# Optimization experiments

Measured on AMD Instinct MI355X. Metric: run time of the kernel, lower is better.

The kernel has to match this reference:

```python
import jax, jax.numpy as jnp
import numpy as np

N, E, D, L, G = 50000, 1600000, 128, 3, 64


def setup_inputs() -> dict:
    key = jax.random.key(0)
    ks = jax.random.split(key, 10)
    s = 1.0 / np.sqrt(D).astype(np.float32)
    X = jax.random.normal(ks[0], (N, D), jnp.float32)
    edge_index = jax.random.randint(ks[1], (2, E), 0, N, dtype=jnp.int32)
    edge_types = jax.random.randint(ks[2], (E,), 0, 2, dtype=jnp.int32)
    batch_ids = jnp.sort(jax.random.randint(ks[3], (N,), 0, G, dtype=jnp.int32))
    Wd = jax.random.uniform(ks[4], (L, D, D), jnp.float32, -s, s)
    bd = jax.random.uniform(ks[5], (L, D), jnp.float32, -s, s)
    Wc = jax.random.uniform(ks[6], (L, D, D), jnp.float32, -s, s)
    bc = jax.random.uniform(ks[7], (L, D), jnp.float32, -s, s)
    Ws = jax.random.uniform(ks[8], (L, D, D), jnp.float32, -s, s)
    bs = jax.random.uniform(ks[9], (L, D), jnp.float32, -s, s)
    return dict(X=X, Wd=Wd, bd=bd, Wc=Wc, bc=bc, Ws=Ws, bs=bs,
                edge_index=edge_index, edge_types=edge_types, batch_ids=batch_ids)


def reference(X, Wd, bd, Wc, bc, Ws, bs, edge_index, edge_types, batch_ids):
    src, dst = edge_index[0], edge_index[1]
    is_data = (edge_types == 0)[:, None]  # [E,1] edge-type selector
    for l in range(L):
        # Linear commutes with gather: compute node-level GEMMs once,
        # then per-edge gather + type select (same math as per-edge Linear).
        Xd = X @ Wd[l] + bd[l]            # [N,D] data-edge messages
        Xc = X @ Wc[l] + bc[l]            # [N,D] control-edge messages
        msg = jnp.where(is_data, Xd[src], Xc[src])      # [E,D]
        agg = jax.ops.segment_sum(msg, dst, num_segments=N)  # scatter-add
        X = jax.nn.relu(agg + X @ Ws[l] + bs[l])
    # global mean pool per graph
    sums = jax.ops.segment_sum(X, batch_ids, num_segments=G)
    cnts = jax.ops.segment_sum(jnp.ones((N,), X.dtype), batch_ids, num_segments=G)
    return sums / jnp.maximum(cnts, 1.0)[:, None]
```

## Files before the change

### kernel.cpp

```cpp
#include <hip/hip_runtime.h>
#include <hip/hip_fp16.h>

#define N_NODES 50000
#define N_EDGES 1600000
#define DIM     128
#define NLAYERS 3
#define NGRAPHS 64

#define NBUCK   196
#define CSR_BLKS 256
#define EPB     (N_EDGES / CSR_BLKS)
#define EITER   ((EPB + 255) / 256)

typedef _Float16 half8 __attribute__((ext_vector_type(8)));
typedef float    f32x4 __attribute__((ext_vector_type(4)));
typedef float    f32x2 __attribute__((ext_vector_type(2)));

#define LDK 136

__device__ __forceinline__ unsigned char f32_to_fp8(float v) {
    int q = __builtin_amdgcn_cvt_pk_fp8_f32(v, v, 0, false);
    return (unsigned char)(q & 0xFF);
}

__global__ __launch_bounds__(256) void setup_kernel(
        const float* __restrict__ X, __half* __restrict__ Xh,
        const float* __restrict__ Wd, const float* __restrict__ Wc,
        const float* __restrict__ Ws, __half* __restrict__ WT,
        float* __restrict__ sums, int* __restrict__ gcnt) {
    int i = blockIdx.x * 256 + threadIdx.x;
    if (i < N_NODES * DIM / 4) {
        float4 v = *(const float4*)(X + (size_t)i * 4);
        union { __half2 h2[2]; uint2 u; } pk;
        pk.h2[0] = __floats2half2_rn(v.x, v.y);
        pk.h2[1] = __floats2half2_rn(v.z, v.w);
        *(uint2*)(Xh + (size_t)i * 4) = pk.u;
    }
    if (i < 9 * DIM * DIM) {
        int k  = i & 127;
        int n  = (i >> 7) & 127;
        int lw = i >> 14;
        int l  = lw / 3, w = lw - 3 * l;
        const float* W = ((w == 0) ? Wd : (w == 1) ? Wc : Ws)
                         + (size_t)l * DIM * DIM;
        WT[i] = __float2half(W[k * DIM + n]);
    }
    if (i < NGRAPHS * DIM) sums[i] = 0.f;
    if (i < NGRAPHS) gcnt[i] = 0;
}

__global__ __launch_bounds__(256) void csr1_kernel(const int* __restrict__ dst,
                                                   int* __restrict__ cntmat) {
    __shared__ int hc[NBUCK];
    int tid = threadIdx.x;
    for (int i = tid; i < NBUCK; i += 256) hc[i] = 0;
    __syncthreads();
    int base = blockIdx.x * EPB;
#pragma unroll
    for (int i = 0; i < EITER; ++i) {
        int idx = i * 256 + tid;
        if (idx < EPB) atomicAdd(&hc[dst[base + idx] >> 8], 1);
    }
    __syncthreads();
    for (int i = tid; i < NBUCK; i += 256)
        cntmat[i * CSR_BLKS + blockIdx.x] = hc[i];
}

__global__ __launch_bounds__(256) void scanA_kernel(const int* __restrict__ cntmat,
                                                    int* __restrict__ exc,
                                                    int* __restrict__ btot) {
    __shared__ int sh[256];
    int tid = threadIdx.x, b = blockIdx.x;
    int v = cntmat[b * CSR_BLKS + tid];
    sh[tid] = v;
    __syncthreads();
    for (int o = 1; o < 256; o <<= 1) {
        int t = (tid >= o) ? sh[tid - o] : 0;
        __syncthreads();
        sh[tid] += t;
        __syncthreads();
    }
    exc[b * CSR_BLKS + tid] = sh[tid] - v;
    if (tid == 255) btot[b] = sh[255];
}

__global__ __launch_bounds__(256) void csr2_kernel(const int* __restrict__ src,
                                                   const int* __restrict__ dst,
                                                   const int* __restrict__ et,
                                                   const int* __restrict__ exc,
                                                   const int* __restrict__ btot,
                                                   int* __restrict__ bstart,
                                                   int* __restrict__ esv) {
    __shared__ int sh[256];
    __shared__ int bst[NBUCK];
    __shared__ int cur[NBUCK];
    int tid = threadIdx.x;
    int v = (tid < NBUCK) ? btot[tid] : 0;
    sh[tid] = v;
    __syncthreads();
    for (int o = 1; o < 256; o <<= 1) {
        int t = (tid >= o) ? sh[tid - o] : 0;
        __syncthreads();
        sh[tid] += t;
        __syncthreads();
    }
    if (tid < NBUCK) bst[tid] = sh[tid] - v;
    if (blockIdx.x == 0) {
        if (tid < NBUCK) bstart[tid] = sh[tid] - v;
        if (tid == NBUCK - 1) bstart[NBUCK] = sh[tid];
    }
    __syncthreads();
    if (tid < NBUCK) cur[tid] = exc[tid * CSR_BLKS + blockIdx.x] + bst[tid];
    __syncthreads();
    int base = blockIdx.x * EPB;
#pragma unroll
    for (int i = 0; i < EITER; ++i) {
        int idx = i * 256 + tid;
        if (idx < EPB) {
            int e = base + idx;
            int d = dst[e];
            int pos = atomicAdd(&cur[d >> 8], 1);
            esv[pos] = (src[e] + et[e] * N_NODES) | ((d & 255) << 17);
        }
    }
}

__global__ __launch_bounds__(256) void csr3_kernel(const int* __restrict__ esv,
                                                   const int* __restrict__ bstart,
                                                   int* __restrict__ col,
                                                   int* __restrict__ row_start,
                                                   int* __restrict__ deg) {
    __shared__ int cnt[256];
    __shared__ int sh[256];
    __shared__ int cur[256];
    int tid = threadIdx.x, b = blockIdx.x;
    int bs = bstart[b], be = bstart[b + 1];
    cnt[tid] = 0;
    __syncthreads();
    for (int e = bs + tid; e < be; e += 256)
        atomicAdd(&cnt[(esv[e] >> 17) & 255], 1);
    __syncthreads();
    int v = cnt[tid];
    sh[tid] = v;
    __syncthreads();
    for (int o = 1; o < 256; o <<= 1) {
        int t = (tid >= o) ? sh[tid - o] : 0;
        __syncthreads();
        sh[tid] += t;
        __syncthreads();
    }
    int off  = sh[tid] - v;
    int node = (b << 8) + tid;
    if (node < N_NODES) {
        row_start[node] = bs + off;
        deg[node]       = v;
    }
    cur[tid] = bs + off;
    __syncthreads();
    for (int e = bs + tid; e < be; e += 256) {
        int pk  = esv[e];
        int nd  = (pk >> 17) & 255;
        int pos = atomicAdd(&cur[nd], 1);
        col[pos] = pk & 0x1FFFF;
    }
}

__global__ __launch_bounds__(256) void gemm3m_kernel(
        const __half* __restrict__ Xh,
        const __half* __restrict__ WTl,
        const float* __restrict__ bd, const float* __restrict__ bc,
        const float* __restrict__ bs,
        unsigned char* __restrict__ Od, unsigned char* __restrict__ Oc,
        __half* __restrict__ Sh) {
    __shared__ _Float16 As[64 * LDK];
    __shared__ _Float16 Bs[128 * LDK];

    const int tid = threadIdx.x;
    const int m0  = blockIdx.x * 64;
    const int w   = blockIdx.y;

#pragma unroll
    for (int i = 0; i < 4; ++i) {
        int c    = i * 256 + tid;
        int row  = c >> 4;
        int colh = (c & 15) * 8;
        uint4 v  = make_uint4(0u, 0u, 0u, 0u);
        int gr   = m0 + row;
        if (gr < N_NODES) v = *(const uint4*)(Xh + (size_t)gr * DIM + colh);
        *(uint4*)(As + row * LDK + colh) = v;
    }
    {
        const __half* Wt = WTl + (size_t)w * DIM * DIM;
#pragma unroll
        for (int i = 0; i < 8; ++i) {
            int c    = i * 256 + tid;
            int row  = c >> 4;
            int colh = (c & 15) * 8;
            uint4 v = *(const uint4*)(Wt + (size_t)row * DIM + colh);
            *(uint4*)(Bs + row * LDK + colh) = v;
        }
    }
    __syncthreads();

    const int wv = tid >> 6;
    const int l  = tid & 63;
    const int lm = l & 15;
    const int q  = l >> 4;

    const float* bias = (w == 0) ? bd : (w == 1) ? bc : bs;
    float b0v = bias[wv * 32 + lm];
    float b1v = bias[wv * 32 + 16 + lm];
    f32x4 acc[4][2];
#pragma unroll
    for (int mt = 0; mt < 4; ++mt) {
        acc[mt][0] = (f32x4){b0v, b0v, b0v, b0v};
        acc[mt][1] = (f32x4){b1v, b1v, b1v, b1v};
    }

#pragma unroll
    for (int ks = 0; ks < 4; ++ks) {
        int coff = ks * 32 + q * 8;
        half8 am[4];
#pragma unroll
        for (int mt = 0; mt < 4; ++mt)
            am[mt] = *(const half8*)(As + (mt * 16 + lm) * LDK + coff);
        half8 bb0 = *(const half8*)(Bs + (wv * 32 + lm) * LDK + coff);
        half8 bb1 = *(const half8*)(Bs + (wv * 32 + 16 + lm) * LDK + coff);
#pragma unroll
        for (int mt = 0; mt < 4; ++mt) {
            acc[mt][0] = __builtin_amdgcn_mfma_f32_16x16x32_f16(am[mt], bb0, acc[mt][0], 0, 0, 0);
            acc[mt][1] = __builtin_amdgcn_mfma_f32_16x16x32_f16(am[mt], bb1, acc[mt][1], 0, 0, 0);
        }
    }

    if (w < 2) {
        unsigned char* O = (w == 0) ? Od : Oc;
#pragma unroll
        for (int mt = 0; mt < 4; ++mt)
#pragma unroll
            for (int nt = 0; nt < 2; ++nt) {
                int colg = wv * 32 + nt * 16 + lm;
#pragma unroll
                for (int r = 0; r < 4; ++r) {
                    int row = m0 + mt * 16 + q * 4 + r;
                    if (row < N_NODES)
                        O[(size_t)row * DIM + colg] = f32_to_fp8(acc[mt][nt][r]);
                }
            }
    } else {
#pragma unroll
        for (int mt = 0; mt < 4; ++mt)
#pragma unroll
            for (int nt = 0; nt < 2; ++nt) {
                int colg = wv * 32 + nt * 16 + lm;
#pragma unroll
                for (int r = 0; r < 4; ++r) {
                    int row = m0 + mt * 16 + q * 4 + r;
                    if (row < N_NODES)
                        Sh[(size_t)row * DIM + colg] = __float2half(acc[mt][nt][r]);
                }
            }
    }
}

__global__ __launch_bounds__(256) void agg_kernel(
        const int* __restrict__ row_start, const int* __restrict__ deg_arr,
        const int* __restrict__ col,
        const unsigned char* __restrict__ Xdc,
        const __half* __restrict__ Sh, __half* __restrict__ Xout) {
    int wave = (blockIdx.x * 256 + threadIdx.x) >> 6;
    int lane = threadIdx.x & 63;
    int half = lane >> 5;
    int l32  = lane & 31;
    int node = wave * 2 + half;
    if (node >= N_NODES) return;

    int rs  = row_start[node];
    int deg = deg_arr[node];
    const size_t off = (size_t)l32 * 4;

    float4 a[8];
#pragma unroll
    for (int i = 0; i < 8; ++i) a[i] = make_float4(0.f, 0.f, 0.f, 0.f);

    if (deg > 0) {
        int dgm1 = deg - 1;
        int nb   = (deg + 7) >> 3;
        for (int b = 0; b < nb; ++b) {
            int e0 = b * 8;
            int p[8];
#pragma unroll
            for (int i = 0; i < 8; ++i) {
                int idx = e0 + i;
                p[i] = col[rs + (idx < deg ? idx : dgm1)];
            }
            unsigned int v[8];
#pragma unroll
            for (int i = 0; i < 8; ++i)
                v[i] = *(const unsigned int*)(Xdc + (size_t)p[i] * DIM + off);
#pragma unroll
            for (int i = 0; i < 8; ++i) {
                if (e0 + i >= deg) v[i] = 0u;
            }
#pragma unroll
            for (int i = 0; i < 8; ++i) {
                f32x2 f0 = __builtin_amdgcn_cvt_pk_f32_fp8(v[i], false);
                f32x2 f1 = __builtin_amdgcn_cvt_pk_f32_fp8(v[i], true);
                a[i].x += f0[0]; a[i].y += f0[1];
                a[i].z += f1[0]; a[i].w += f1[1];
            }
        }
    }

#pragma unroll
    for (int i = 1; i < 8; ++i) {
        a[0].x += a[i].x; a[0].y += a[i].y;
        a[0].z += a[i].z; a[0].w += a[i].w;
    }

    union { uint2 u; __half2 h2[2]; } sv;
    sv.u = *(const uint2*)(Sh + (size_t)node * DIM + off);
    float2 s0 = __half22float2(sv.h2[0]);
    float2 s1 = __half22float2(sv.h2[1]);

    float rx = fmaxf(a[0].x + s0.x, 0.f);
    float ry = fmaxf(a[0].y + s0.y, 0.f);
    float rz = fmaxf(a[0].z + s1.x, 0.f);
    float rw = fmaxf(a[0].w + s1.y, 0.f);

    union { __half2 h2[2]; uint2 u; } pk;
    pk.h2[0] = __floats2half2_rn(rx, ry);
    pk.h2[1] = __floats2half2_rn(rz, rw);
    *(uint2*)(Xout + (size_t)node * DIM + off) = pk.u;
}

__global__ __launch_bounds__(256) void pool_kernel(const __half* __restrict__ X,
                                                   const int* __restrict__ bid,
                                                   float* __restrict__ sums,
                                                   int* __restrict__ gcnt) {
    __shared__ float acc[8][DIM];
    __shared__ int scnt[8];
    __shared__ int sgmin;
    int tid = threadIdx.x;
    for (int i = tid; i < 8 * DIM; i += 256) ((float*)acc)[i] = 0.f;
    if (tid < 8) scnt[tid] = 0;
    int n0 = blockIdx.x * 64;
    if (tid == 0) sgmin = bid[n0];
    __syncthreads();
    int gmin = sgmin;

    int s    = tid >> 5;
    int lane = tid & 31;
    int r0   = n0 + s * 8;

    int g[8];
    union { uint2 u; __half2 h2[2]; } v[8];
#pragma unroll
    for (int i = 0; i < 8; ++i) {
        int r = r0 + i;
        g[i] = (r < N_NODES) ? bid[r] : -1;
    }
#pragma unroll
    for (int i = 0; i < 8; ++i) {
        int r = r0 + i;
        if (r < N_NODES)
            v[i].u = *(const uint2*)(X + (size_t)r * DIM + lane * 4);
        else { v[i].u.x = 0u; v[i].u.y = 0u; }
    }

    float4 a = make_float4(0.f, 0.f, 0.f, 0.f);
    int cur = -1, run = 0;
#pragma unroll
    for (int i = 0; i < 8; ++i) {
        if (g[i] != cur) {
            if (cur >= 0) {
                int slot = cur - gmin;
                if (slot < 8) {
                    atomicAdd(&acc[slot][lane * 4 + 0], a.x);
                    atomicAdd(&acc[slot][lane * 4 + 1], a.y);
                    atomicAdd(&acc[slot][lane * 4 + 2], a.z);
                    atomicAdd(&acc[slot][lane * 4 + 3], a.w);
                    if (lane == 0) atomicAdd(&scnt[slot], run);
                } else {
                    atomicAdd(&sums[cur * DIM + lane * 4 + 0], a.x);
                    atomicAdd(&sums[cur * DIM + lane * 4 + 1], a.y);
                    atomicAdd(&sums[cur * DIM + lane * 4 + 2], a.z);
                    atomicAdd(&sums[cur * DIM + lane * 4 + 3], a.w);
                    if (lane == 0) atomicAdd(&gcnt[cur], run);
                }
            }
            cur = g[i];
            a = make_float4(0.f, 0.f, 0.f, 0.f);
            run = 0;
        }
        if (g[i] >= 0) {
            float2 f0 = __half22float2(v[i].h2[0]);
            float2 f1 = __half22float2(v[i].h2[1]);
            a.x += f0.x; a.y += f0.y; a.z += f1.x; a.w += f1.y;
            run++;
        }
    }
    if (cur >= 0) {
        int slot = cur - gmin;
        if (slot < 8) {
            atomicAdd(&acc[slot][lane * 4 + 0], a.x);
            atomicAdd(&acc[slot][lane * 4 + 1], a.y);
            atomicAdd(&acc[slot][lane * 4 + 2], a.z);
            atomicAdd(&acc[slot][lane * 4 + 3], a.w);
            if (lane == 0) atomicAdd(&scnt[slot], run);
        } else {
            atomicAdd(&sums[cur * DIM + lane * 4 + 0], a.x);
            atomicAdd(&sums[cur * DIM + lane * 4 + 1], a.y);
            atomicAdd(&sums[cur * DIM + lane * 4 + 2], a.z);
            atomicAdd(&sums[cur * DIM + lane * 4 + 3], a.w);
            if (lane == 0) atomicAdd(&gcnt[cur], run);
        }
    }
    __syncthreads();

    for (int slot = 0; slot < 8; ++slot) {
        if (scnt[slot] > 0) {
            int gg = gmin + slot;
            for (int i = tid; i < DIM; i += 256)
                atomicAdd(&sums[gg * DIM + i], acc[slot][i]);
            if (tid == 0) atomicAdd(&gcnt[gg], scnt[slot]);
        }
    }
}

__global__ __launch_bounds__(256) void div_kernel(const float* __restrict__ sums,
                                                  const int* __restrict__ gcnt,
                                                  float* __restrict__ out) {
    int i = blockIdx.x * 256 + threadIdx.x;
    if (i < NGRAPHS * DIM) {
        int g = i >> 7;
        out[i] = sums[i] / fmaxf((float)gcnt[g], 1.f);
    }
}

extern "C" void kernel_launch(void* const* d_in, const int* in_sizes, int n_in,
                              void* d_out, int out_size, void* d_ws, size_t ws_size,
                              hipStream_t stream) {
    const float* Xin = (const float*)d_in[0];
    const float* Wd  = (const float*)d_in[1];
    const float* bd  = (const float*)d_in[2];
    const float* Wc  = (const float*)d_in[3];
    const float* bc  = (const float*)d_in[4];
    const float* Ws  = (const float*)d_in[5];
    const float* bs  = (const float*)d_in[6];
    const int* edge_index = (const int*)d_in[7];
    const int* edge_types = (const int*)d_in[8];
    const int* batch_ids  = (const int*)d_in[9];

    const int* src = edge_index;
    const int* dst = edge_index + N_EDGES;

    const size_t NBH = (size_t)N_NODES * DIM * sizeof(__half);
    const size_t NB8 = (size_t)N_NODES * DIM;
    char* w = (char*)d_ws;
    auto take = [&](size_t bytes) {
        char* p = w;
        w += (bytes + 255) & ~(size_t)255;
        return p;
    };
    __half* X0h  = (__half*)take(NBH);
    __half* Xb0h = (__half*)take(NBH);
    __half* Xb1h = (__half*)take(NBH);
    unsigned char* Xdc = (unsigned char*)take(2 * NB8);
    __half* Shb  = (__half*)take(NBH);
    __half* WT   = (__half*)take((size_t)9 * DIM * DIM * sizeof(__half));
    int* col     = (int*)take((size_t)N_EDGES * 4);
    int* esv     = (int*)take((size_t)N_EDGES * 4);
    int* cntmat  = (int*)take((size_t)NBUCK * CSR_BLKS * 4);
    int* exc     = (int*)take((size_t)NBUCK * CSR_BLKS * 4);
    int* btot    = (int*)take((size_t)NBUCK * 4);
    int* bstart  = (int*)take((size_t)(NBUCK + 1) * 4);
    int* rowst   = (int*)take((size_t)N_NODES * 4);
    int* deg     = (int*)take((size_t)N_NODES * 4);
    float* sums  = (float*)take((size_t)NGRAPHS * DIM * 4);
    int* gcnt    = (int*)take(NGRAPHS * 4);

    setup_kernel<<<(N_NODES * DIM / 4 + 255) / 256, 256, 0, stream>>>(
        Xin, X0h, Wd, Wc, Ws, WT, sums, gcnt);

    csr1_kernel<<<CSR_BLKS, 256, 0, stream>>>(dst, cntmat);
    scanA_kernel<<<NBUCK, 256, 0, stream>>>(cntmat, exc, btot);
    csr2_kernel<<<CSR_BLKS, 256, 0, stream>>>(src, dst, edge_types, exc,
                                              btot, bstart, esv);
    csr3_kernel<<<NBUCK, 256, 0, stream>>>(esv, bstart, col, rowst, deg);

    const int GEMM_MBLK = (N_NODES + 63) / 64;
    const int AGG_BLKS  = (N_NODES / 2 + 3) / 4;
    const __half* Xcur = X0h;
    __half* bufs[3] = {Xb0h, Xb1h, Xb0h};
    for (int l = 0; l < NLAYERS; ++l) {
        gemm3m_kernel<<<dim3(GEMM_MBLK, 3), 256, 0, stream>>>(
            Xcur, WT + (size_t)l * 3 * DIM * DIM,
            bd + (size_t)l * DIM, bc + (size_t)l * DIM, bs + (size_t)l * DIM,
            Xdc, Xdc + NB8, Shb);
        __half* Xnext = bufs[l];
        agg_kernel<<<AGG_BLKS, 256, 0, stream>>>(rowst, deg, col, Xdc, Shb, Xnext);
        Xcur = Xnext;
    }

    const int POOL_BLKS = (N_NODES + 63) / 64;
    pool_kernel<<<POOL_BLKS, 256, 0, stream>>>(Xcur, batch_ids, sums, gcnt);
    div_kernel<<<(NGRAPHS * DIM + 255) / 256, 256, 0, stream>>>(sums, gcnt,
                                                                (float*)d_out);
}
```

Measured before the change: 323.5 us.

## Process four nodes per wave with 8-byte fp8 gathers and prefetched indices

The aggregation kernel now assigns 16 lanes per node, so each wave handles four nodes instead of two. Each lane gathers 8 fp8 values per neighbor row instead of 4, and stores with 16-byte writes. The next block of neighbor indices is loaded while the current rows are being gathered, to hide index-load latency. In exchange, each lane needs more registers, and the eight-wide unroll now feeds a single shared set of accumulators, which creates a serial dependency chain.

```diff
diff --git a/kernel.cpp b/kernel.cpp
--- a/kernel.cpp
+++ b/kernel.cpp
@@ -270,68 +270,82 @@
         const __half* __restrict__ Sh, __half* __restrict__ Xout) {
     int wave = (blockIdx.x * 256 + threadIdx.x) >> 6;
     int lane = threadIdx.x & 63;
-    int half = lane >> 5;
-    int l32  = lane & 31;
-    int node = wave * 2 + half;
+    int grp  = lane >> 4;
+    int l16  = lane & 15;
+    int node = wave * 4 + grp;
     if (node >= N_NODES) return;
 
     int rs  = row_start[node];
     int deg = deg_arr[node];
-    const size_t off = (size_t)l32 * 4;
-
-    float4 a[8];
-#pragma unroll
-    for (int i = 0; i < 8; ++i) a[i] = make_float4(0.f, 0.f, 0.f, 0.f);
+    const size_t off = (size_t)l16 * 8;
+
+    union { uint4 u; __half2 h2[4]; } sv;
+    sv.u = *(const uint4*)(Sh + (size_t)node * DIM + off);
+
+    float acc[8];
+#pragma unroll
+    for (int j = 0; j < 8; ++j) acc[j] = 0.f;
 
     if (deg > 0) {
         int dgm1 = deg - 1;
         int nb   = (deg + 7) >> 3;
+        int p[8];
+#pragma unroll
+        for (int i = 0; i < 8; ++i)
+            p[i] = col[rs + (i < deg ? i : dgm1)];
         for (int b = 0; b < nb; ++b) {
             int e0 = b * 8;
-            int p[8];
+            uint2 v[8];
+#pragma unroll
+            for (int i = 0; i < 8; ++i)
+                v[i] = *(const uint2*)(Xdc + (size_t)p[i] * DIM + off);
+            int pn[8];
+            if (b + 1 < nb) {
+                int e1 = e0 + 8;
+#pragma unroll
+                for (int i = 0; i < 8; ++i) {
+                    int idx = e1 + i;
+                    pn[i] = col[rs + (idx < deg ? idx : dgm1)];
+                }
+            }
 #pragma unroll
             for (int i = 0; i < 8; ++i) {
-                int idx = e0 + i;
-                p[i] = col[rs + (idx < deg ? idx : dgm1)];
-            }
-            unsigned int v[8];
-#pragma unroll
-            for (int i = 0; i < 8; ++i)
-                v[i] = *(const unsigned int*)(Xdc + (size_t)p[i] * DIM + off);
+                if (e0 + i >= deg) { v[i].x = 0u; v[i].y = 0u; }
+            }
 #pragma unroll
             for (int i = 0; i < 8; ++i) {
-                if (e0 + i >= deg) v[i] = 0u;
-            }
-#pragma unroll
-            for (int i = 0; i < 8; ++i) {
-                f32x2 f0 = __builtin_amdgcn_cvt_pk_f32_fp8(v[i], false);
-                f32x2 f1 = __builtin_amdgcn_cvt_pk_f32_fp8(v[i], true);
-                a[i].x += f0[0]; a[i].y += f0[1];
-                a[i].z += f1[0]; a[i].w += f1[1];
-            }
-        }
-    }
-
-#pragma unroll
-    for (int i = 1; i < 8; ++i) {
-        a[0].x += a[i].x; a[0].y += a[i].y;
-        a[0].z += a[i].z; a[0].w += a[i].w;
-    }
-
-    union { uint2 u; __half2 h2[2]; } sv;
-    sv.u = *(const uint2*)(Sh + (size_t)node * DIM + off);
-    float2 s0 = __half22float2(sv.h2[0]);
-    float2 s1 = __half22float2(sv.h2[1]);
-
-    float rx = fmaxf(a[0].x + s0.x, 0.f);
-    float ry = fmaxf(a[0].y + s0.y, 0.f);
-    float rz = fmaxf(a[0].z + s1.x, 0.f);
-    float rw = fmaxf(a[0].w + s1.y, 0.f);
-
-    union { __half2 h2[2]; uint2 u; } pk;
-    pk.h2[0] = __floats2half2_rn(rx, ry);
-    pk.h2[1] = __floats2half2_rn(rz, rw);
-    *(uint2*)(Xout + (size_t)node * DIM + off) = pk.u;
+                f32x2 f0 = __builtin_amdgcn_cvt_pk_f32_fp8(v[i].x, false);
+                f32x2 f1 = __builtin_amdgcn_cvt_pk_f32_fp8(v[i].x, true);
+                f32x2 f2 = __builtin_amdgcn_cvt_pk_f32_fp8(v[i].y, false);
+                f32x2 f3 = __builtin_amdgcn_cvt_pk_f32_fp8(v[i].y, true);
+                acc[0] += f0[0]; acc[1] += f0[1];
+                acc[2] += f1[0]; acc[3] += f1[1];
+                acc[4] += f2[0]; acc[5] += f2[1];
+                acc[6] += f3[0]; acc[7] += f3[1];
+            }
+            if (b + 1 < nb) {
+#pragma unroll
+                for (int i = 0; i < 8; ++i) p[i] = pn[i];
+            }
+        }
+    }
+
+    float s[8];
+#pragma unroll
+    for (int j = 0; j < 4; ++j) {
+        float2 f = __half22float2(sv.h2[j]);
+        s[2 * j]     = f.x;
+        s[2 * j + 1] = f.y;
+    }
+
+    union { __half2 h2[4]; uint4 u; } pk;
+#pragma unroll
+    for (int j = 0; j < 4; ++j) {
+        float r0 = fmaxf(acc[2 * j]     + s[2 * j],     0.f);
+        float r1 = fmaxf(acc[2 * j + 1] + s[2 * j + 1], 0.f);
+        pk.h2[j] = __floats2half2_rn(r0, r1);
+    }
+    *(uint4*)(Xout + (size_t)node * DIM + off) = pk.u;
 }
 
 __global__ __launch_bounds__(256) void pool_kernel(const __half* __restrict__ X,
@@ -490,7 +504,7 @@
     csr3_kernel<<<NBUCK, 256, 0, stream>>>(esv, bstart, col, rowst, deg);
 
     const int GEMM_MBLK = (N_NODES + 63) / 64;
-    const int AGG_BLKS  = (N_NODES / 2 + 3) / 4;
+    const int AGG_BLKS  = (N_NODES + 15) / 16;
     const __half* Xcur = X0h;
     __half* bufs[3] = {Xb0h, Xb1h, Xb0h};
     for (int l = 0; l < NLAYERS; ++l) {
```

New measurement: 307.2 us. 5.1% less time.
